# Kernel tuning notes

Hardware: AMD Instinct MI355X
Metric: run time of the kernel (lower is better)

The kernel has to match this reference:

```python
import jax, jax.numpy as jnp
import numpy as np
import math

B, S, D = 4, 1024, 512
H, DK, DV = 8, 64, 64
NEG = -1.0e9
LN_EPS = 1e-5


def setup_inputs() -> dict:
    key = jax.random.key(0)
    ks = jax.random.split(key, 12)
    sc = 1.0 / math.sqrt(D)
    inp = {
        "input_Q": jax.random.normal(ks[0], (B, S, D), jnp.float32),
        "input_K": jax.random.normal(ks[1], (B, S, D), jnp.float32),
        "input_V": jax.random.normal(ks[2], (B, S, D), jnp.float32),
        "attn_mask": jax.random.randint(ks[3], (B, S, S), 0, 2).astype(bool),
        "bias_mask": jax.random.randint(ks[4], (B, S, S), 0, 2).astype(bool),
        "Wq": jax.random.normal(ks[5], (D, H * DK), jnp.float32) * sc,
        "Wk": jax.random.normal(ks[6], (D, H * DK), jnp.float32) * sc,
        "Wq2": jax.random.normal(ks[7], (D, H * DK), jnp.float32) * sc,
        "Wk2": jax.random.normal(ks[8], (D, H * DK), jnp.float32) * sc,
        "Wv": jax.random.normal(ks[9], (D, H * DV), jnp.float32) * sc,
        "Wo": jax.random.normal(ks[10], (H * DV, D), jnp.float32) * sc,
        "ln_g": jnp.ones((D,), jnp.float32),
        "ln_b": jnp.zeros((D,), jnp.float32),
    }
    return inp


def _heads(x, W, d):
    b, s, _ = x.shape
    return (x @ W).reshape(b, s, H, d).transpose(0, 2, 1, 3)  # [B,H,S,d]


def reference(input_Q, input_K, input_V, attn_mask, bias_mask,
              Wq, Wk, Wq2, Wk2, Wv, Wo, ln_g, ln_b):
    residual = input_Q
    Q = _heads(input_Q, Wq, DK)
    K = _heads(input_K, Wk, DK)
    V = _heads(input_V, Wv, DV)
    Q2 = _heads(input_Q, Wq2, DK)
    K2 = _heads(input_K, Wk2, DK)

    am = attn_mask[:, None, :, :]   # broadcast over heads
    bm = bias_mask[:, None, :, :]

    scores1 = jnp.einsum('bhqd,bhkd->bhqk', Q, K) / math.sqrt(DK)
    bias = jnp.einsum('bhqd,bhkd->bhqk', Q2, K2)
    bias = jnp.where(bm, NEG, bias)
    scores = jnp.where(am, NEG, scores1 + bias)
    attn = jax.nn.softmax(scores, axis=-1)          # [B,H,S,S]
    context = jnp.einsum('bhqk,bhkd->bhqd', attn, V)  # [B,H,S,DV]
    context = context.transpose(0, 2, 1, 3).reshape(B, S, H * DV)
    output = context @ Wo

    x = output + residual
    mu = jnp.mean(x, axis=-1, keepdims=True)
    var = jnp.mean(jnp.square(x - mu), axis=-1, keepdims=True)
    out = (x - mu) / jnp.sqrt(var + LN_EPS) * ln_g + ln_b
    return (out, attn)
```

## Files before the change

### kernel.cpp

```cpp
#include <hip/hip_runtime.h>
#include <hip/hip_fp16.h>

typedef _Float16 f16x8 __attribute__((ext_vector_type(8)));
typedef _Float16 f16x4 __attribute__((ext_vector_type(4)));
typedef float f32x4 __attribute__((ext_vector_type(4)));

__global__ __launch_bounds__(256) void wtrans6_kernel(
    const float* __restrict__ Wq, const float* __restrict__ Wk,
    const float* __restrict__ Wq2, const float* __restrict__ Wk2,
    const float* __restrict__ Wv, const float* __restrict__ Wo,
    __half* __restrict__ WqcT, __half* __restrict__ WkcT,
    __half* __restrict__ WvT, __half* __restrict__ WoT) {
  const float* src;
  __half* dst;
  float scale = 1.0f;
  switch (blockIdx.z) {
    case 0: src = Wq;  dst = WqcT;              scale = 0.125f; break;
    case 1: src = Wq2; dst = WqcT + 512 * 512;  break;
    case 2: src = Wk;  dst = WkcT;              break;
    case 3: src = Wk2; dst = WkcT + 512 * 512;  break;
    case 4: src = Wv;  dst = WvT;               break;
    default: src = Wo; dst = WoT;               break;
  }
  __shared__ float t[32][33];
  int n0 = blockIdx.x * 32, k0 = blockIdx.y * 32;
  int tx = threadIdx.x, ty = threadIdx.y;
#pragma unroll
  for (int i = 0; i < 4; i++)
    t[ty + i * 8][tx] = src[(size_t)(k0 + ty + i * 8) * 512 + n0 + tx];
  __syncthreads();
#pragma unroll
  for (int i = 0; i < 4; i++)
    dst[(size_t)(n0 + ty + i * 8) * 512 + k0 + tx] = __float2half(t[tx][ty + i * 8] * scale);
}

__device__ __forceinline__ void maskprep_body(const int* __restrict__ am,
                                              const int* __restrict__ bm,
                                              uint32_t* __restrict__ packed, int bk,
                                              int t) {
  int w = bk & 3, bqt = bk >> 2, qt = bqt & 31, b = bqt >> 5;
  int mi = t >> 6, lane = t & 63;
  int lg = lane >> 4, l15 = lane & 15;
  int qbase = qt * 32 + mi * 16 + lg * 4;
  int kbase = w * 256 + l15;
  uint32_t outw[4] = {0u, 0u, 0u, 0u};
#pragma unroll
  for (int kt = 0; kt < 16; kt++) {
    int k = kbase + kt * 16;
#pragma unroll
    for (int r = 0; r < 4; r++) {
      size_t idx = ((size_t)(b * 1024 + qbase + r)) * 1024 + k;
      uint32_t code = (am[idx] ? 1u : 0u) + (bm[idx] ? 1u : 0u);
      outw[kt >> 2] |= code << (((kt & 3) << 3) + (r << 1));
    }
  }
  uint4* dst = (uint4*)packed + ((size_t)bk * 64 + lane) * 2 + mi;
  *dst = make_uint4(outw[0], outw[1], outw[2], outw[3]);
}

template <int AF32>
__device__ __forceinline__ void gemm_body(const void* Ap, const __half* Bt, __half* C,
                                          int N, int bx, int by, int vt,
                                          __half* __restrict__ vtp) {
  __shared__ __align__(16) _Float16 smem[10240];
  _Float16(*As)[40] = (_Float16(*)[40])smem;
  _Float16(*Bs)[40] = (_Float16(*)[40])(smem + 5120);
  int tid = threadIdx.x;
  int wave = tid >> 6, lane = tid & 63;
  int lg = lane >> 4, l15 = lane & 15;
  int wm = (wave >> 1) * 64, wn = (wave & 1) * 64;
  int bm0 = by * 128, bn0 = bx * 128;
  int srow = tid >> 1, sseg = (tid & 1) * 16;
  const float* Af = (const float*)Ap;
  const __half* Ah = (const __half*)Ap;
  f32x4 acc[4][4];
#pragma unroll
  for (int i = 0; i < 4; i++)
#pragma unroll
    for (int j = 0; j < 4; j++) acc[i][j] = (f32x4){0.f, 0.f, 0.f, 0.f};

  for (int kt = 0; kt < 16; kt++) {
    int k0 = kt * 32;
    if (AF32) {
      const float* s = Af + (size_t)(bm0 + srow) * 512 + k0 + sseg;
      _Float16* d = &As[srow][sseg];
#pragma unroll
      for (int i = 0; i < 16; i += 4) {
        float4 v = *(const float4*)(s + i);
        d[i] = (_Float16)v.x; d[i + 1] = (_Float16)v.y;
        d[i + 2] = (_Float16)v.z; d[i + 3] = (_Float16)v.w;
      }
    } else {
      const __half* s = Ah + (size_t)(bm0 + srow) * 512 + k0 + sseg;
      *(uint4*)&As[srow][sseg] = *(const uint4*)s;
      *(uint4*)(&As[srow][sseg] + 8) = *(const uint4*)(s + 8);
    }
    {
      const __half* s = Bt + (size_t)(bn0 + srow) * 512 + k0 + sseg;
      *(uint4*)&Bs[srow][sseg] = *(const uint4*)s;
      *(uint4*)(&Bs[srow][sseg] + 8) = *(const uint4*)(s + 8);
    }
    __syncthreads();
    f16x8 af[4], bf[4];
#pragma unroll
    for (int i = 0; i < 4; i++) af[i] = *(const f16x8*)&As[wm + i * 16 + l15][lg * 8];
#pragma unroll
    for (int j = 0; j < 4; j++) bf[j] = *(const f16x8*)&Bs[wn + j * 16 + l15][lg * 8];
#pragma unroll
    for (int i = 0; i < 4; i++)
#pragma unroll
      for (int j = 0; j < 4; j++)
        acc[i][j] = __builtin_amdgcn_mfma_f32_16x16x32_f16(af[i], bf[j], acc[i][j], 0, 0, 0);
    __syncthreads();
  }

  _Float16* cb = smem;
#pragma unroll
  for (int ph = 0; ph < 2; ph++) {
    __syncthreads();
    if ((wave >> 1) == ph) {
#pragma unroll
      for (int i = 0; i < 4; i++)
#pragma unroll
        for (int j = 0; j < 4; j++)
#pragma unroll
          for (int r = 0; r < 4; r++)
            cb[(i * 16 + lg * 4 + r) * 128 + wn + j * 16 + l15] =
                (_Float16)acc[i][j][r];
    }
    __syncthreads();
    if (!vt) {
#pragma unroll
      for (int rr = 0; rr < 4; rr++) {
        int row = rr * 16 + (tid >> 4);
        int colh = (tid & 15) * 8;
        uint4 v = *(const uint4*)&cb[row * 128 + colh];
        *(uint4*)&C[(size_t)(bm0 + ph * 64 + row) * N + bn0 + colh] = v;
      }
    } else {
      int m0 = bm0 + ph * 64;
      int b = m0 >> 10, s0 = m0 & 1023;
      int dvc = tid >> 1;
      int sh = tid & 1;
      int bh = b * 8 + bx * 2 + (dvc >> 6);
      int dv = dvc & 63;
      __half* dst = vtp + ((size_t)bh * 64 + dv) * 1024 + s0 + sh * 32;
#pragma unroll
      for (int g = 0; g < 4; g++) {
        f16x8 v;
#pragma unroll
        for (int k = 0; k < 8; k++) v[k] = cb[(sh * 32 + g * 8 + k) * 128 + dvc];
        *(f16x8*)(dst + g * 8) = v;
      }
    }
  }
}

__global__ __launch_bounds__(256) void proj_kernel(
    const float* __restrict__ inQ, const float* __restrict__ inK,
    const float* __restrict__ inV, const __half* __restrict__ WqcT,
    const __half* __restrict__ WkcT, const __half* __restrict__ WvT,
    const int* __restrict__ am, const int* __restrict__ bm,
    __half* __restrict__ QQ2, __half* __restrict__ KK2, __half* __restrict__ Vt,
    uint32_t* __restrict__ packed) {
  int z = blockIdx.z;
  if (z == 0) {
    gemm_body<1>(inQ, WqcT, QQ2, 1024, blockIdx.x, blockIdx.y, 0, nullptr);
  } else if (z == 1) {
    gemm_body<1>(inK, WkcT, KK2, 1024, blockIdx.x, blockIdx.y, 0, nullptr);
  } else if (z == 2) {
    if (blockIdx.x >= 4) return;
    gemm_body<1>(inV, WvT, nullptr, 512, blockIdx.x, blockIdx.y, 1, Vt);
  } else {
    int bk = (blockIdx.y * 8 + blockIdx.x) * 2 + (threadIdx.x >> 7);
    maskprep_body(am, bm, packed, bk, threadIdx.x & 127);
  }
}

__global__ __launch_bounds__(256) void gemm_f16_kernel(const __half* __restrict__ A,
                                                       const __half* __restrict__ Bt,
                                                       __half* __restrict__ C, int N) {
  gemm_body<0>(A, Bt, C, N, blockIdx.x, blockIdx.y, 0, nullptr);
}

__global__ __launch_bounds__(256, 2) void attn_kernel(
    const __half* __restrict__ QQ2, const __half* __restrict__ KK2,
    const __half* __restrict__ Vt, const uint32_t* __restrict__ packed,
    float* __restrict__ attn_out, __half* __restrict__ CTX) {
  int qt = blockIdx.x, bh = blockIdx.y;
  int b = bh >> 3, h = bh & 7;
  int q0 = qt * 32;
  int tid = threadIdx.x;
  int wave = tid >> 6, lane = tid & 63;
  int lg = lane >> 4, l15 = lane & 15;
  int kw = wave * 256;

  __shared__ __align__(16) _Float16 P[4][32][264];
  __shared__ float redmax[4][32], redsum[4][32];

  f16x8 qf[2][4];
  const __half* Qb = QQ2 + ((size_t)(b * 1024 + q0)) * 1024 + h * 64;
#pragma unroll
  for (int mi = 0; mi < 2; mi++)
#pragma unroll
    for (int ks = 0; ks < 4; ks++) {
      int off = (ks < 2) ? ks * 32 : 512 + (ks - 2) * 32;
      qf[mi][ks] = *(const f16x8*)(Qb + (size_t)(mi * 16 + l15) * 1024 + off + lg * 8);
    }

  uint4 mw[2];
  {
    const uint4* mp =
        (const uint4*)packed + ((size_t)((b * 32 + qt) * 4 + wave) * 64 + lane) * 2;
    mw[0] = mp[0];
    mw[1] = mp[1];
  }

  f16x4 sc16[2][16];
  float mx[2][4];
#pragma unroll
  for (int mi = 0; mi < 2; mi++)
#pragma unroll
    for (int r = 0; r < 4; r++) mx[mi][r] = -3.0e38f;
  const __half* Kb = KK2 + ((size_t)(b * 1024)) * 1024 + h * 64;
#pragma unroll
  for (int kt = 0; kt < 16; kt++) {
    int kc = kw + kt * 16;
    const __half* kp = Kb + (size_t)(kc + l15) * 1024 + lg * 8;
    f16x8 kf[4];
    kf[0] = *(const f16x8*)kp;
    kf[1] = *(const f16x8*)(kp + 32);
    kf[2] = *(const f16x8*)(kp + 512);
    kf[3] = *(const f16x8*)(kp + 544);
#pragma unroll
    for (int mi = 0; mi < 2; mi++) {
      f32x4 s = (f32x4){0.f, 0.f, 0.f, 0.f};
#pragma unroll
      for (int ks = 0; ks < 4; ks++)
        s = __builtin_amdgcn_mfma_f32_16x16x32_f16(qf[mi][ks], kf[ks], s, 0, 0, 0);
      uint32_t mword = ((const uint32_t*)&mw[mi])[kt >> 2];
      f16x4 sv;
#pragma unroll
      for (int r = 0; r < 4; r++) {
        uint32_t code = (mword >> (((kt & 3) << 3) + (r << 1))) & 3u;
        float sval = s[r] - 30000.0f * (float)code;
        sv[r] = (_Float16)sval;
        mx[mi][r] = fmaxf(mx[mi][r], (float)sv[r]);
      }
      sc16[mi][kt] = sv;
    }
  }

#pragma unroll
  for (int mi = 0; mi < 2; mi++)
#pragma unroll
    for (int r = 0; r < 4; r++) {
      float m = mx[mi][r];
#pragma unroll
      for (int o = 1; o < 16; o <<= 1) m = fmaxf(m, __shfl_xor(m, o));
      if (l15 == 0) redmax[wave][mi * 16 + lg * 4 + r] = m;
    }
  __syncthreads();
  float mfin[2][4];
#pragma unroll
  for (int mi = 0; mi < 2; mi++)
#pragma unroll
    for (int r = 0; r < 4; r++) {
      int row = mi * 16 + lg * 4 + r;
      mfin[mi][r] = fmaxf(fmaxf(redmax[0][row], redmax[1][row]),
                          fmaxf(redmax[2][row], redmax[3][row]));
    }

  float sm[2][4];
#pragma unroll
  for (int mi = 0; mi < 2; mi++)
#pragma unroll
    for (int r = 0; r < 4; r++) sm[mi][r] = 0.f;
#pragma unroll
  for (int kt = 0; kt < 16; kt++)
#pragma unroll
    for (int mi = 0; mi < 2; mi++) {
      f16x4 sv = sc16[mi][kt];
      f16x4 pv;
#pragma unroll
      for (int r = 0; r < 4; r++) {
        float p = __expf((float)sv[r] - mfin[mi][r]);
        sm[mi][r] += p;
        pv[r] = (_Float16)p;
      }
      sc16[mi][kt] = pv;
    }
#pragma unroll
  for (int mi = 0; mi < 2; mi++)
#pragma unroll
    for (int r = 0; r < 4; r++) {
      float s = sm[mi][r];
#pragma unroll
      for (int o = 1; o < 16; o <<= 1) s += __shfl_xor(s, o);
      if (l15 == 0) redsum[wave][mi * 16 + lg * 4 + r] = s;
    }
  __syncthreads();
  float inv[2][4];
#pragma unroll
  for (int mi = 0; mi < 2; mi++)
#pragma unroll
    for (int r = 0; r < 4; r++) {
      int row = mi * 16 + lg * 4 + r;
      inv[mi][r] =
          1.0f / (redsum[0][row] + redsum[1][row] + redsum[2][row] + redsum[3][row]);
    }

  float* ab = attn_out + ((size_t)bh * 1024 + q0) * 1024;
#pragma unroll
  for (int mi = 0; mi < 2; mi++)
#pragma unroll
    for (int kt = 0; kt < 16; kt++)
#pragma unroll
      for (int r = 0; r < 4; r++) {
        int row = mi * 16 + lg * 4 + r;
        int col = kw + kt * 16 + l15;
        float a = (float)sc16[mi][kt][r] * inv[mi][r];
        ab[(size_t)row * 1024 + col] = a;
        P[wave][row][kt * 16 + l15] = (_Float16)a;
      }
  __syncthreads();

  f32x4 ctx[2];
  ctx[0] = (f32x4){0.f, 0.f, 0.f, 0.f};
  ctx[1] = (f32x4){0.f, 0.f, 0.f, 0.f};
  const __half* Vb = Vt + (size_t)bh * 64 * 1024;
#pragma unroll
  for (int c = 0; c < 4; c++) {
    int kglob = c * 256;
#pragma unroll
    for (int kk = 0; kk < 8; kk++) {
      f16x8 pa0 = *(const f16x8*)&P[c][l15][kk * 32 + lg * 8];
      f16x8 pa1 = *(const f16x8*)&P[c][16 + l15][kk * 32 + lg * 8];
      f16x8 vf = *(const f16x8*)(Vb + (size_t)(wave * 16 + l15) * 1024 + kglob +
                                 kk * 32 + lg * 8);
      ctx[0] = __builtin_amdgcn_mfma_f32_16x16x32_f16(pa0, vf, ctx[0], 0, 0, 0);
      ctx[1] = __builtin_amdgcn_mfma_f32_16x16x32_f16(pa1, vf, ctx[1], 0, 0, 0);
    }
  }

#pragma unroll
  for (int mi = 0; mi < 2; mi++)
#pragma unroll
    for (int r = 0; r < 4; r++) {
      int row = mi * 16 + lg * 4 + r;
      CTX[(size_t)(b * 1024 + q0 + row) * 512 + h * 64 + wave * 16 + l15] =
          __float2half(ctx[mi][r]);
    }
}

__global__ __launch_bounds__(256) void ln_kernel(const __half* __restrict__ O,
                                                 const float* __restrict__ resid,
                                                 const float* __restrict__ g,
                                                 const float* __restrict__ bb,
                                                 float* __restrict__ out) {
  int w = threadIdx.x >> 6, lane = threadIdx.x & 63;
  int row = blockIdx.x * 4 + w;
  size_t base = (size_t)row * 512 + lane * 8;
  f16x8 ov = *(const f16x8*)(O + base);
  float4 r0 = *(const float4*)(resid + base);
  float4 r1 = *(const float4*)(resid + base + 4);
  float x[8];
  x[0] = (float)ov[0] + r0.x; x[1] = (float)ov[1] + r0.y;
  x[2] = (float)ov[2] + r0.z; x[3] = (float)ov[3] + r0.w;
  x[4] = (float)ov[4] + r1.x; x[5] = (float)ov[5] + r1.y;
  x[6] = (float)ov[6] + r1.z; x[7] = (float)ov[7] + r1.w;
  float s = 0.f;
#pragma unroll
  for (int i = 0; i < 8; i++) s += x[i];
#pragma unroll
  for (int o = 1; o < 64; o <<= 1) s += __shfl_xor(s, o);
  float mean = s * (1.0f / 512.0f);
  float d[8], v = 0.f;
#pragma unroll
  for (int i = 0; i < 8; i++) { d[i] = x[i] - mean; v += d[i] * d[i]; }
#pragma unroll
  for (int o = 1; o < 64; o <<= 1) v += __shfl_xor(v, o);
  float rs = rsqrtf(v * (1.0f / 512.0f) + 1e-5f);
  float4 g0 = *(const float4*)(g + lane * 8);
  float4 g1 = *(const float4*)(g + lane * 8 + 4);
  float4 b0 = *(const float4*)(bb + lane * 8);
  float4 b1 = *(const float4*)(bb + lane * 8 + 4);
  f32x4 o0 = {d[0] * rs * g0.x + b0.x, d[1] * rs * g0.y + b0.y,
              d[2] * rs * g0.z + b0.z, d[3] * rs * g0.w + b0.w};
  f32x4 o1 = {d[4] * rs * g1.x + b1.x, d[5] * rs * g1.y + b1.y,
              d[6] * rs * g1.z + b1.z, d[7] * rs * g1.w + b1.w};
  __builtin_nontemporal_store(o0, (f32x4*)(out + base));
  __builtin_nontemporal_store(o1, (f32x4*)(out + base + 4));
}

extern "C" void kernel_launch(void* const* d_in, const int* in_sizes, int n_in,
                              void* d_out, int out_size, void* d_ws, size_t ws_size,
                              hipStream_t stream) {
  const float* inQ = (const float*)d_in[0];
  const float* inK = (const float*)d_in[1];
  const float* inV = (const float*)d_in[2];
  const int* am = (const int*)d_in[3];
  const int* bmk = (const int*)d_in[4];
  const float* Wq = (const float*)d_in[5];
  const float* Wk = (const float*)d_in[6];
  const float* Wq2 = (const float*)d_in[7];
  const float* Wk2 = (const float*)d_in[8];
  const float* Wv = (const float*)d_in[9];
  const float* Wo = (const float*)d_in[10];
  const float* lng = (const float*)d_in[11];
  const float* lnb = (const float*)d_in[12];

  char* ws = (char*)d_ws;
  __half* WqcT = (__half*)ws; ws += (size_t)1024 * 512 * 2;
  __half* WkcT = (__half*)ws; ws += (size_t)1024 * 512 * 2;
  __half* WvT = (__half*)ws;  ws += (size_t)512 * 512 * 2;
  __half* WoT = (__half*)ws;  ws += (size_t)512 * 512 * 2;
  __half* QQ2 = (__half*)ws;  ws += (size_t)4096 * 1024 * 2;
  __half* KK2 = (__half*)ws;  ws += (size_t)4096 * 1024 * 2;
  __half* Vt = (__half*)ws;   ws += (size_t)4096 * 512 * 2;
  __half* CTX = (__half*)ws;  ws += (size_t)4096 * 512 * 2;
  __half* Obuf = (__half*)ws; ws += (size_t)4096 * 512 * 2;
  uint32_t* packed = (uint32_t*)Obuf;

  float* out0 = (float*)d_out;
  float* attn_out = out0 + (size_t)4 * 1024 * 512;

  wtrans6_kernel<<<dim3(16, 16, 6), dim3(32, 8), 0, stream>>>(Wq, Wk, Wq2, Wk2, Wv, Wo,
                                                              WqcT, WkcT, WvT, WoT);
  proj_kernel<<<dim3(8, 32, 4), 256, 0, stream>>>(inQ, inK, inV, WqcT, WkcT, WvT, am,
                                                  bmk, QQ2, KK2, Vt, packed);
  attn_kernel<<<dim3(32, 32), 256, 0, stream>>>(QQ2, KK2, Vt, packed, attn_out, CTX);
  gemm_f16_kernel<<<dim3(4, 32), 256, 0, stream>>>(CTX, WoT, Obuf, 512);
  ln_kernel<<<1024, 256, 0, stream>>>(Obuf, inQ, lng, lnb, out0);
}
```

Baseline: 138.3 us.

## Split attention key range across eight waves per block with split-K PV reduction

Raises the attention block from 4 to 8 waves, so each wave covers 128 keys instead of 256. The packed-mask layout and the mask prep kernel are changed to match. The P·V stage now splits the key dimension across two halves of the waves and adds the partial context through LDS. The aim is to cut per-wave register pressure and raise the number of waves in flight, at the cost of more shared memory per block, an extra barrier, and extra reduction traffic.

```diff
diff --git a/kernel.cpp b/kernel.cpp
--- a/kernel.cpp
+++ b/kernel.cpp
@@ -38,14 +38,14 @@
                                               const int* __restrict__ bm,
                                               uint32_t* __restrict__ packed, int bk,
                                               int t) {
-  int w = bk & 3, bqt = bk >> 2, qt = bqt & 31, b = bqt >> 5;
+  int w = bk & 7, bqt = bk >> 3, qt = bqt & 31, b = bqt >> 5;
   int mi = t >> 6, lane = t & 63;
   int lg = lane >> 4, l15 = lane & 15;
   int qbase = qt * 32 + mi * 16 + lg * 4;
-  int kbase = w * 256 + l15;
-  uint32_t outw[4] = {0u, 0u, 0u, 0u};
-#pragma unroll
-  for (int kt = 0; kt < 16; kt++) {
+  int kbase = w * 128 + l15;
+  uint32_t outw[2] = {0u, 0u};
+#pragma unroll
+  for (int kt = 0; kt < 8; kt++) {
     int k = kbase + kt * 16;
 #pragma unroll
     for (int r = 0; r < 4; r++) {
@@ -54,8 +54,8 @@
       outw[kt >> 2] |= code << (((kt & 3) << 3) + (r << 1));
     }
   }
-  uint4* dst = (uint4*)packed + ((size_t)bk * 64 + lane) * 2 + mi;
-  *dst = make_uint4(outw[0], outw[1], outw[2], outw[3]);
+  uint2* dst = (uint2*)packed + ((size_t)bk * 64 + lane) * 2 + mi;
+  *dst = make_uint2(outw[0], outw[1]);
 }
 
 template <int AF32>
@@ -172,8 +172,11 @@
     if (blockIdx.x >= 4) return;
     gemm_body<1>(inV, WvT, nullptr, 512, blockIdx.x, blockIdx.y, 1, Vt);
   } else {
-    int bk = (blockIdx.y * 8 + blockIdx.x) * 2 + (threadIdx.x >> 7);
-    maskprep_body(am, bm, packed, bk, threadIdx.x & 127);
+    int base = (blockIdx.y * 8 + blockIdx.x) * 4;
+    int sub = threadIdx.x >> 7;
+    int t = threadIdx.x & 127;
+    maskprep_body(am, bm, packed, base + sub, t);
+    maskprep_body(am, bm, packed, base + 2 + sub, t);
   }
 }
 
@@ -183,7 +186,7 @@
   gemm_body<0>(A, Bt, C, N, blockIdx.x, blockIdx.y, 0, nullptr);
 }
 
-__global__ __launch_bounds__(256, 2) void attn_kernel(
+__global__ __launch_bounds__(512, 4) void attn_kernel(
     const __half* __restrict__ QQ2, const __half* __restrict__ KK2,
     const __half* __restrict__ Vt, const uint32_t* __restrict__ packed,
     float* __restrict__ attn_out, __half* __restrict__ CTX) {
@@ -193,10 +196,11 @@
   int tid = threadIdx.x;
   int wave = tid >> 6, lane = tid & 63;
   int lg = lane >> 4, l15 = lane & 15;
-  int kw = wave * 256;
-
-  __shared__ __align__(16) _Float16 P[4][32][264];
-  __shared__ float redmax[4][32], redsum[4][32];
+  int kw = wave * 128;
+
+  __shared__ __align__(16) _Float16 P[32][1032];
+  __shared__ float redmax[8][32], redsum[8][32];
+  __shared__ float cred[32][66];
 
   f16x8 qf[2][4];
   const __half* Qb = QQ2 + ((size_t)(b * 1024 + q0)) * 1024 + h * 64;
@@ -208,15 +212,15 @@
       qf[mi][ks] = *(const f16x8*)(Qb + (size_t)(mi * 16 + l15) * 1024 + off + lg * 8);
     }
 
-  uint4 mw[2];
+  uint2 mw[2];
   {
-    const uint4* mp =
-        (const uint4*)packed + ((size_t)((b * 32 + qt) * 4 + wave) * 64 + lane) * 2;
+    const uint2* mp =
+        (const uint2*)packed + ((size_t)((b * 32 + qt) * 8 + wave) * 64 + lane) * 2;
     mw[0] = mp[0];
     mw[1] = mp[1];
   }
 
-  f16x4 sc16[2][16];
+  f16x4 sc16[2][8];
   float mx[2][4];
 #pragma unroll
   for (int mi = 0; mi < 2; mi++)
@@ -224,7 +228,7 @@
     for (int r = 0; r < 4; r++) mx[mi][r] = -3.0e38f;
   const __half* Kb = KK2 + ((size_t)(b * 1024)) * 1024 + h * 64;
 #pragma unroll
-  for (int kt = 0; kt < 16; kt++) {
+  for (int kt = 0; kt < 8; kt++) {
     int kc = kw + kt * 16;
     const __half* kp = Kb + (size_t)(kc + l15) * 1024 + lg * 8;
     f16x8 kf[4];
@@ -238,7 +242,7 @@
 #pragma unroll
       for (int ks = 0; ks < 4; ks++)
         s = __builtin_amdgcn_mfma_f32_16x16x32_f16(qf[mi][ks], kf[ks], s, 0, 0, 0);
-      uint32_t mword = ((const uint32_t*)&mw[mi])[kt >> 2];
+      uint32_t mword = (kt < 4) ? mw[mi].x : mw[mi].y;
       f16x4 sv;
 #pragma unroll
       for (int r = 0; r < 4; r++) {
@@ -267,8 +271,11 @@
 #pragma unroll
     for (int r = 0; r < 4; r++) {
       int row = mi * 16 + lg * 4 + r;
-      mfin[mi][r] = fmaxf(fmaxf(redmax[0][row], redmax[1][row]),
-                          fmaxf(redmax[2][row], redmax[3][row]));
+      float m0 = fmaxf(fmaxf(redmax[0][row], redmax[1][row]),
+                       fmaxf(redmax[2][row], redmax[3][row]));
+      float m1 = fmaxf(fmaxf(redmax[4][row], redmax[5][row]),
+                       fmaxf(redmax[6][row], redmax[7][row]));
+      mfin[mi][r] = fmaxf(m0, m1);
     }
 
   float sm[2][4];
@@ -277,7 +284,7 @@
 #pragma unroll
     for (int r = 0; r < 4; r++) sm[mi][r] = 0.f;
 #pragma unroll
-  for (int kt = 0; kt < 16; kt++)
+  for (int kt = 0; kt < 8; kt++)
 #pragma unroll
     for (int mi = 0; mi < 2; mi++) {
       f16x4 sv = sc16[mi][kt];
@@ -306,51 +313,60 @@
 #pragma unroll
     for (int r = 0; r < 4; r++) {
       int row = mi * 16 + lg * 4 + r;
-      inv[mi][r] =
-          1.0f / (redsum[0][row] + redsum[1][row] + redsum[2][row] + redsum[3][row]);
+      inv[mi][r] = 1.0f / (redsum[0][row] + redsum[1][row] + redsum[2][row] +
+                           redsum[3][row] + redsum[4][row] + redsum[5][row] +
+                           redsum[6][row] + redsum[7][row]);
     }
 
   float* ab = attn_out + ((size_t)bh * 1024 + q0) * 1024;
 #pragma unroll
   for (int mi = 0; mi < 2; mi++)
 #pragma unroll
-    for (int kt = 0; kt < 16; kt++)
+    for (int kt = 0; kt < 8; kt++)
 #pragma unroll
       for (int r = 0; r < 4; r++) {
         int row = mi * 16 + lg * 4 + r;
         int col = kw + kt * 16 + l15;
         float a = (float)sc16[mi][kt][r] * inv[mi][r];
         ab[(size_t)row * 1024 + col] = a;
-        P[wave][row][kt * 16 + l15] = (_Float16)a;
+        P[row][col] = (_Float16)a;
       }
   __syncthreads();
 
+  int kh = wave >> 2;
+  int dvw = (wave & 3) * 16;
   f32x4 ctx[2];
   ctx[0] = (f32x4){0.f, 0.f, 0.f, 0.f};
   ctx[1] = (f32x4){0.f, 0.f, 0.f, 0.f};
-  const __half* Vb = Vt + (size_t)bh * 64 * 1024;
-#pragma unroll
-  for (int c = 0; c < 4; c++) {
-    int kglob = c * 256;
-#pragma unroll
-    for (int kk = 0; kk < 8; kk++) {
-      f16x8 pa0 = *(const f16x8*)&P[c][l15][kk * 32 + lg * 8];
-      f16x8 pa1 = *(const f16x8*)&P[c][16 + l15][kk * 32 + lg * 8];
-      f16x8 vf = *(const f16x8*)(Vb + (size_t)(wave * 16 + l15) * 1024 + kglob +
-                                 kk * 32 + lg * 8);
-      ctx[0] = __builtin_amdgcn_mfma_f32_16x16x32_f16(pa0, vf, ctx[0], 0, 0, 0);
-      ctx[1] = __builtin_amdgcn_mfma_f32_16x16x32_f16(pa1, vf, ctx[1], 0, 0, 0);
-    }
-  }
-
-#pragma unroll
-  for (int mi = 0; mi < 2; mi++)
-#pragma unroll
-    for (int r = 0; r < 4; r++) {
-      int row = mi * 16 + lg * 4 + r;
-      CTX[(size_t)(b * 1024 + q0 + row) * 512 + h * 64 + wave * 16 + l15] =
-          __float2half(ctx[mi][r]);
-    }
+  const __half* Vb = Vt + (size_t)bh * 64 * 1024 + kh * 512;
+  const _Float16* Pb = &P[0][kh * 512];
+#pragma unroll
+  for (int kk = 0; kk < 16; kk++) {
+    f16x8 pa0 = *(const f16x8*)(Pb + (size_t)l15 * 1032 + kk * 32 + lg * 8);
+    f16x8 pa1 = *(const f16x8*)(Pb + (size_t)(16 + l15) * 1032 + kk * 32 + lg * 8);
+    f16x8 vf = *(const f16x8*)(Vb + (size_t)(dvw + l15) * 1024 + kk * 32 + lg * 8);
+    ctx[0] = __builtin_amdgcn_mfma_f32_16x16x32_f16(pa0, vf, ctx[0], 0, 0, 0);
+    ctx[1] = __builtin_amdgcn_mfma_f32_16x16x32_f16(pa1, vf, ctx[1], 0, 0, 0);
+  }
+  if (kh == 1) {
+#pragma unroll
+    for (int mi = 0; mi < 2; mi++)
+#pragma unroll
+      for (int r = 0; r < 4; r++)
+        cred[mi * 16 + lg * 4 + r][dvw + l15] = ctx[mi][r];
+  }
+  __syncthreads();
+  if (kh == 0) {
+#pragma unroll
+    for (int mi = 0; mi < 2; mi++)
+#pragma unroll
+      for (int r = 0; r < 4; r++) {
+        int row = mi * 16 + lg * 4 + r;
+        float v = ctx[mi][r] + cred[row][dvw + l15];
+        CTX[(size_t)(b * 1024 + q0 + row) * 512 + h * 64 + dvw + l15] =
+            __float2half(v);
+      }
+  }
 }
 
 __global__ __launch_bounds__(256) void ln_kernel(const __half* __restrict__ O,
@@ -429,7 +445,7 @@
                                                               WqcT, WkcT, WvT, WoT);
   proj_kernel<<<dim3(8, 32, 4), 256, 0, stream>>>(inQ, inK, inV, WqcT, WkcT, WvT, am,
                                                   bmk, QQ2, KK2, Vt, packed);
-  attn_kernel<<<dim3(32, 32), 256, 0, stream>>>(QQ2, KK2, Vt, packed, attn_out, CTX);
+  attn_kernel<<<dim3(32, 32), 512, 0, stream>>>(QQ2, KK2, Vt, packed, attn_out, CTX);
   gemm_f16_kernel<<<dim3(4, 32), 256, 0, stream>>>(CTX, WoT, Obuf, 512);
   ln_kernel<<<1024, 256, 0, stream>>>(Obuf, inQ, lng, lnb, out0);
 }
```

Result: slower. 147.4 us (+6.6%).

## Store K and V projections in MFMA fragment-packed layout for coalesced attention loads

Applied to the files above, without the earlier changes.

The projection GEMM epilogue now writes K/K2 and V directly in a per-lane MFMA fragment order, so each attention wave reads one contiguous 16-byte chunk per lane instead of strided rows. It also pads the epilogue shared-memory staging buffer stride from 128 to 136 halves to reduce LDS bank conflicts in the transposing writes. The aim is better coalescing of the K and V global loads in the attention kernel. In exchange the projection epilogue does more scattered LDS reads, and the staging buffer now needs 64x136 halves, which must still fit inside the existing shared array.

```diff
diff --git a/kernel.cpp b/kernel.cpp
--- a/kernel.cpp
+++ b/kernel.cpp
@@ -58,10 +58,10 @@
   *dst = make_uint4(outw[0], outw[1], outw[2], outw[3]);
 }
 
-template <int AF32>
+template <int AF32, int MODE>
 __device__ __forceinline__ void gemm_body(const void* Ap, const __half* Bt, __half* C,
-                                          int N, int bx, int by, int vt,
-                                          __half* __restrict__ vtp) {
+                                          int N, int bx, int by,
+                                          __half* __restrict__ pk) {
   __shared__ __align__(16) _Float16 smem[10240];
   _Float16(*As)[40] = (_Float16(*)[40])smem;
   _Float16(*Bs)[40] = (_Float16(*)[40])(smem + 5120);
@@ -125,32 +125,47 @@
         for (int j = 0; j < 4; j++)
 #pragma unroll
           for (int r = 0; r < 4; r++)
-            cb[(i * 16 + lg * 4 + r) * 128 + wn + j * 16 + l15] =
+            cb[(i * 16 + lg * 4 + r) * 136 + wn + j * 16 + l15] =
                 (_Float16)acc[i][j][r];
     }
     __syncthreads();
-    if (!vt) {
+    if (MODE == 0) {
 #pragma unroll
       for (int rr = 0; rr < 4; rr++) {
         int row = rr * 16 + (tid >> 4);
         int colh = (tid & 15) * 8;
-        uint4 v = *(const uint4*)&cb[row * 128 + colh];
+        uint4 v = *(const uint4*)&cb[row * 136 + colh];
         *(uint4*)&C[(size_t)(bm0 + ph * 64 + row) * N + bn0 + colh] = v;
+      }
+    } else if (MODE == 2) {
+      int m0 = bm0 + ph * 64;
+      int b = m0 >> 10;
+      int kblk0 = (m0 & 1023) >> 4;
+      int isK2 = (bn0 >= 512) ? 1 : 0;
+      int hpair = (isK2 ? (bx - 4) : bx) * 2;
+      int sel = tid >> 6;
+      int hh = sel >> 1, ksl = sel & 1;
+      int bh = b * 8 + hpair + hh;
+      int ksd = isK2 * 2 + ksl;
+#pragma unroll
+      for (int kb = 0; kb < 4; kb++) {
+        f16x8 v = *(const f16x8*)&cb[(kb * 16 + l15) * 136 + hh * 64 + ksl * 32 + lg * 8];
+        *(f16x8*)(pk + ((((size_t)bh * 64 + kblk0 + kb) * 4 + ksd) * 64 + lane) * 8) = v;
       }
     } else {
       int m0 = bm0 + ph * 64;
-      int b = m0 >> 10, s0 = m0 & 1023;
-      int dvc = tid >> 1;
-      int sh = tid & 1;
-      int bh = b * 8 + bx * 2 + (dvc >> 6);
-      int dv = dvc & 63;
-      __half* dst = vtp + ((size_t)bh * 64 + dv) * 1024 + s0 + sh * 32;
-#pragma unroll
-      for (int g = 0; g < 4; g++) {
+      int b = m0 >> 10;
+      int k320 = (m0 & 1023) >> 5;
+      int sel = tid >> 6;
+      int hh = sel >> 1, kk2 = sel & 1;
+      int bh = b * 8 + bx * 2 + hh;
+#pragma unroll
+      for (int dvb = 0; dvb < 4; dvb++) {
         f16x8 v;
 #pragma unroll
-        for (int k = 0; k < 8; k++) v[k] = cb[(sh * 32 + g * 8 + k) * 128 + dvc];
-        *(f16x8*)(dst + g * 8) = v;
+        for (int j = 0; j < 8; j++)
+          v[j] = cb[(kk2 * 32 + lg * 8 + j) * 136 + hh * 64 + dvb * 16 + l15];
+        *(f16x8*)(pk + ((((size_t)bh * 32 + k320 + kk2) * 4 + dvb) * 64 + lane) * 8) = v;
       }
     }
   }
@@ -161,16 +176,16 @@
     const float* __restrict__ inV, const __half* __restrict__ WqcT,
     const __half* __restrict__ WkcT, const __half* __restrict__ WvT,
     const int* __restrict__ am, const int* __restrict__ bm,
-    __half* __restrict__ QQ2, __half* __restrict__ KK2, __half* __restrict__ Vt,
+    __half* __restrict__ QQ2, __half* __restrict__ Kpk, __half* __restrict__ Vpk,
     uint32_t* __restrict__ packed) {
   int z = blockIdx.z;
   if (z == 0) {
-    gemm_body<1>(inQ, WqcT, QQ2, 1024, blockIdx.x, blockIdx.y, 0, nullptr);
+    gemm_body<1, 0>(inQ, WqcT, QQ2, 1024, blockIdx.x, blockIdx.y, nullptr);
   } else if (z == 1) {
-    gemm_body<1>(inK, WkcT, KK2, 1024, blockIdx.x, blockIdx.y, 0, nullptr);
+    gemm_body<1, 2>(inK, WkcT, nullptr, 1024, blockIdx.x, blockIdx.y, Kpk);
   } else if (z == 2) {
     if (blockIdx.x >= 4) return;
-    gemm_body<1>(inV, WvT, nullptr, 512, blockIdx.x, blockIdx.y, 1, Vt);
+    gemm_body<1, 1>(inV, WvT, nullptr, 512, blockIdx.x, blockIdx.y, Vpk);
   } else {
     int bk = (blockIdx.y * 8 + blockIdx.x) * 2 + (threadIdx.x >> 7);
     maskprep_body(am, bm, packed, bk, threadIdx.x & 127);
@@ -180,12 +195,12 @@
 __global__ __launch_bounds__(256) void gemm_f16_kernel(const __half* __restrict__ A,
                                                        const __half* __restrict__ Bt,
                                                        __half* __restrict__ C, int N) {
-  gemm_body<0>(A, Bt, C, N, blockIdx.x, blockIdx.y, 0, nullptr);
+  gemm_body<0, 0>(A, Bt, C, N, blockIdx.x, blockIdx.y, nullptr);
 }
 
 __global__ __launch_bounds__(256, 2) void attn_kernel(
-    const __half* __restrict__ QQ2, const __half* __restrict__ KK2,
-    const __half* __restrict__ Vt, const uint32_t* __restrict__ packed,
+    const __half* __restrict__ QQ2, const __half* __restrict__ Kpk,
+    const __half* __restrict__ Vpk, const uint32_t* __restrict__ packed,
     float* __restrict__ attn_out, __half* __restrict__ CTX) {
   int qt = blockIdx.x, bh = blockIdx.y;
   int b = bh >> 3, h = bh & 7;
@@ -222,16 +237,15 @@
   for (int mi = 0; mi < 2; mi++)
 #pragma unroll
     for (int r = 0; r < 4; r++) mx[mi][r] = -3.0e38f;
-  const __half* Kb = KK2 + ((size_t)(b * 1024)) * 1024 + h * 64;
+  const __half* Kbp = Kpk + ((size_t)bh * 64 + wave * 16) * 4 * 512 + lane * 8;
 #pragma unroll
   for (int kt = 0; kt < 16; kt++) {
-    int kc = kw + kt * 16;
-    const __half* kp = Kb + (size_t)(kc + l15) * 1024 + lg * 8;
+    const __half* kp = Kbp + (size_t)kt * 4 * 512;
     f16x8 kf[4];
     kf[0] = *(const f16x8*)kp;
-    kf[1] = *(const f16x8*)(kp + 32);
-    kf[2] = *(const f16x8*)(kp + 512);
-    kf[3] = *(const f16x8*)(kp + 544);
+    kf[1] = *(const f16x8*)(kp + 512);
+    kf[2] = *(const f16x8*)(kp + 1024);
+    kf[3] = *(const f16x8*)(kp + 1536);
 #pragma unroll
     for (int mi = 0; mi < 2; mi++) {
       f32x4 s = (f32x4){0.f, 0.f, 0.f, 0.f};
@@ -328,16 +342,15 @@
   f32x4 ctx[2];
   ctx[0] = (f32x4){0.f, 0.f, 0.f, 0.f};
   ctx[1] = (f32x4){0.f, 0.f, 0.f, 0.f};
-  const __half* Vb = Vt + (size_t)bh * 64 * 1024;
+  const __half* Vbp = Vpk + ((size_t)bh * 32 * 4 + wave) * 512 + lane * 8;
 #pragma unroll
   for (int c = 0; c < 4; c++) {
-    int kglob = c * 256;
 #pragma unroll
     for (int kk = 0; kk < 8; kk++) {
+      int k32 = c * 8 + kk;
       f16x8 pa0 = *(const f16x8*)&P[c][l15][kk * 32 + lg * 8];
       f16x8 pa1 = *(const f16x8*)&P[c][16 + l15][kk * 32 + lg * 8];
-      f16x8 vf = *(const f16x8*)(Vb + (size_t)(wave * 16 + l15) * 1024 + kglob +
-                                 kk * 32 + lg * 8);
+      f16x8 vf = *(const f16x8*)(Vbp + (size_t)k32 * 4 * 512);
       ctx[0] = __builtin_amdgcn_mfma_f32_16x16x32_f16(pa0, vf, ctx[0], 0, 0, 0);
       ctx[1] = __builtin_amdgcn_mfma_f32_16x16x32_f16(pa1, vf, ctx[1], 0, 0, 0);
     }
@@ -416,8 +429,8 @@
   __half* WvT = (__half*)ws;  ws += (size_t)512 * 512 * 2;
   __half* WoT = (__half*)ws;  ws += (size_t)512 * 512 * 2;
   __half* QQ2 = (__half*)ws;  ws += (size_t)4096 * 1024 * 2;
-  __half* KK2 = (__half*)ws;  ws += (size_t)4096 * 1024 * 2;
-  __half* Vt = (__half*)ws;   ws += (size_t)4096 * 512 * 2;
+  __half* Kpk = (__half*)ws;  ws += (size_t)4096 * 1024 * 2;
+  __half* Vpk = (__half*)ws;  ws += (size_t)4096 * 512 * 2;
   __half* CTX = (__half*)ws;  ws += (size_t)4096 * 512 * 2;
   __half* Obuf = (__half*)ws; ws += (size_t)4096 * 512 * 2;
   uint32_t* packed = (uint32_t*)Obuf;
@@ -428,8 +441,8 @@
   wtrans6_kernel<<<dim3(16, 16, 6), dim3(32, 8), 0, stream>>>(Wq, Wk, Wq2, Wk2, Wv, Wo,
                                                               WqcT, WkcT, WvT, WoT);
   proj_kernel<<<dim3(8, 32, 4), 256, 0, stream>>>(inQ, inK, inV, WqcT, WkcT, WvT, am,
-                                                  bmk, QQ2, KK2, Vt, packed);
-  attn_kernel<<<dim3(32, 32), 256, 0, stream>>>(QQ2, KK2, Vt, packed, attn_out, CTX);
+                                                  bmk, QQ2, Kpk, Vpk, packed);
+  attn_kernel<<<dim3(32, 32), 256, 0, stream>>>(QQ2, Kpk, Vpk, packed, attn_out, CTX);
   gemm_f16_kernel<<<dim3(4, 32), 256, 0, stream>>>(CTX, WoT, Obuf, 512);
   ln_kernel<<<1024, 256, 0, stream>>>(Obuf, inQ, lng, lnb, out0);
 }
```

Result: faster. 127.6 us (-7.7%).
